# Performance work log

Hardware: AMD Instinct MI355X
Metric: run time of the kernel (lower is better)

The kernel has to match this reference:

```python
import jax, jax.numpy as jnp
import numpy as np

KAPPA = 10000.0
B_CONST = 0.5


def pe_matrix(L, dim):
    # pe[j,i] = sin(j/kappa^(i/dim)) for even i, cos(j/kappa^((i-1)/dim)) for odd i
    j = jnp.arange(L, dtype=jnp.float32)[:, None]
    i = jnp.arange(dim, dtype=jnp.float32)[None, :]
    even = (jnp.arange(dim) % 2 == 0)[None, :]
    expo = jnp.where(even, i, i - 1.0) / dim
    ang = j / (KAPPA ** expo)
    return jnp.where(even, jnp.sin(ang), jnp.cos(ang))  # [L, dim]


def setup_inputs() -> dict:
    key = jax.random.key(0)
    ks = jax.random.split(key, 6)
    B, N, L, d, n = 4, 8, 1024, 256, 3
    theta = jax.random.normal(ks[0], (B, N, L, d), dtype=jnp.float32)
    xi = jax.random.normal(ks[1], (B, N, L, n), dtype=jnp.float32)
    edge_attr = jax.random.normal(ks[2], (B, L, N * (N - 1) * 2), dtype=jnp.float32)
    s = 1.0 / np.sqrt(d)
    Wq = jax.random.normal(ks[3], (d, d), dtype=jnp.float32) * s
    Wk = jax.random.normal(ks[4], (d, d), dtype=jnp.float32) * s
    Wv = jax.random.normal(ks[5], (d, d), dtype=jnp.float32) * s
    return {"theta": theta, "xi": xi, "edge_attr": edge_attr, "Wq": Wq, "Wk": Wk, "Wv": Wv}


def reference(theta, xi, edge_attr, Wq, Wk, Wv):
    B, N, L, d = theta.shape
    n = xi.shape[-1]
    # positional encoding (dropout in eval mode = identity)
    theta = theta + pe_matrix(L, d)
    xi = xi + pe_matrix(L, n)
    edge_attr = edge_attr + pe_matrix(L, N * (N - 1) * 2)[None]

    causal = jnp.triu(jnp.ones((L, L), dtype=bool), 1)  # True above diagonal
    neg_inf = jnp.float32(-jnp.inf)

    # feature path: standard causal scaled-dot-product attention
    q = jnp.einsum('bnld,ed->bnle', theta, Wq)
    k = jnp.einsum('bnld,ed->bnle', theta, Wk)
    v = jnp.einsum('bnld,ed->bnle', theta, Wv)
    scores = jnp.einsum('bnqd,bnkd->bnqk', q, k) / jnp.sqrt(jnp.float32(d))
    scores = jnp.where(causal, neg_inf, scores)
    h_out = jnp.einsum('bnqk,bnkd->bnqd', jax.nn.softmax(scores, axis=-1), v)

    # equivariant path: pairwise squared-distance attention
    D = xi[:, :, :, None, :] - xi[:, :, None, :, :]  # [B,N,L,L,n]
    sq = jnp.sum(D * D, axis=-1)                     # [B,N,L,L]
    sq = jnp.where(causal, neg_inf, sq)
    beta = jax.nn.softmax(sq, axis=-1)
    mbeta = beta * (1.0 - jnp.eye(L, dtype=beta.dtype))  # zero the diagonal
    second = B_CONST * jnp.einsum('bnqk,bnkc->bnqc', mbeta, xi)
    third = B_CONST * jnp.sum(mbeta, axis=-1, keepdims=True) * xi
    x_out = xi + second - third

    return h_out, x_out, edge_attr
```

## Files before the change

kernel.cpp:

```cpp
#include <hip/hip_runtime.h>
#include <math.h>

#define L    1024
#define D    256
#define NCH  3
#define HEADS 32
#define EDIM 112
#define BATCH 4

typedef __bf16 bf8_t __attribute__((ext_vector_type(8)));
typedef float  f4_t  __attribute__((ext_vector_type(4)));

typedef __attribute__((address_space(1))) const void GVC;
typedef __attribute__((address_space(3))) void LDSV;

__device__ inline unsigned short f2bf(float x) {
    unsigned u = __float_as_uint(x);
    u += 0x7FFFu + ((u >> 16) & 1u);
    return (unsigned short)(u >> 16);
}
__device__ inline float bf2f(unsigned short h) {
    return __uint_as_float(((unsigned)h) << 16);
}

__global__ void prep_kernel(const float* __restrict__ edge, const float* __restrict__ xi,
                            float* __restrict__ pe_d, float* __restrict__ eout,
                            float* __restrict__ xsb)
{
    int idx = blockIdx.x * blockDim.x + threadIdx.x;
    if (idx < L * D) {
        int l = idx >> 8, i = idx & (D - 1);
        float expo = (float)(i & ~1) * (1.0f / (float)D);
        float ang = (float)l * __powf(10000.0f, -expo);
        pe_d[idx] = (i & 1) ? cosf(ang) : sinf(ang);
    } else if (idx < L * D + BATCH * L * EDIM) {
        int j = idx - L * D;
        int i = j % EDIM;
        int l = (j / EDIM) % L;
        float expo = (float)(i & ~1) * (1.0f / (float)EDIM);
        float ang = (float)l * __powf(10000.0f, -expo);
        eout[j] = edge[j] + ((i & 1) ? cosf(ang) : sinf(ang));
    } else {
        int j = idx - (L * D + BATCH * L * EDIM);
        if (j < HEADS * L * NCH) {
            int c = j % 3;
            int l = (j / 3) & (L - 1);
            float ang = (c == 2) ? (float)l * 0.0021544347f : (float)l;
            float pe = (c == 1) ? cosf(ang) : sinf(ang);
            xsb[j] = xi[j] + pe;
        }
    }
}

__global__ __launch_bounds__(256) void qkv_mfma(
    const float* __restrict__ theta, const float* __restrict__ pe_d,
    const float* __restrict__ Wq, const float* __restrict__ Wk, const float* __restrict__ Wv,
    unsigned short* __restrict__ qh, unsigned short* __restrict__ ql,
    unsigned short* __restrict__ kh, unsigned short* __restrict__ vt)
{
    __shared__ unsigned short XsH[128][40], XsL[128][40], WsH[128][40];

    int tid = threadIdx.x;
    int w = tid >> 6, lane = tid & 63;
    int quad = lane >> 4, l16 = lane & 15;
    int aoff = (w & 1) * 64, boff = (w >> 1) * 64;

    int b = blockIdx.x;
    int xcd = b & 7, r = b >> 3;
    int bx = r % 6;
    int rowPanel = (r / 6) * 8 + xcd;
    int rowBase = rowPanel * 128;
    int wsel = bx >> 1;
    int eBase = (bx & 1) * 128;
    const float* W = (wsel == 0) ? Wq : (wsel == 1) ? Wk : Wv;

    f4_t acc[4][4];
    #pragma unroll
    for (int mi = 0; mi < 4; mi++)
        #pragma unroll
        for (int ni = 0; ni < 4; ni++) acc[mi][ni] = (f4_t){0.f, 0.f, 0.f, 0.f};

    int sr = tid >> 1;
    int ks = (tid & 1) * 16;

    for (int kt = 0; kt < 8; kt++) {
        int k0 = kt * 32 + ks;
        __syncthreads();
        {
            union { unsigned short us[16]; float4 f4[2]; } hi, lo;
            const float* tp = &theta[(size_t)(rowBase + sr) * D + k0];
            const float* pp = &pe_d[(size_t)((rowBase + sr) & (L - 1)) * D + k0];
            #pragma unroll
            for (int j = 0; j < 4; j++) {
                float4 tv = reinterpret_cast<const float4*>(tp)[j];
                float4 pv = reinterpret_cast<const float4*>(pp)[j];
                float xs[4] = {tv.x + pv.x, tv.y + pv.y, tv.z + pv.z, tv.w + pv.w};
                #pragma unroll
                for (int q = 0; q < 4; q++) {
                    unsigned short h = f2bf(xs[q]);
                    hi.us[j * 4 + q] = h;
                    lo.us[j * 4 + q] = f2bf(xs[q] - bf2f(h));
                }
            }
            *reinterpret_cast<float4*>(&XsH[sr][ks]) = hi.f4[0];
            *reinterpret_cast<float4*>(&XsH[sr][ks + 8]) = hi.f4[1];
            *reinterpret_cast<float4*>(&XsL[sr][ks]) = lo.f4[0];
            *reinterpret_cast<float4*>(&XsL[sr][ks + 8]) = lo.f4[1];

            const float* wp = &W[(size_t)(eBase + sr) * D + k0];
            #pragma unroll
            for (int j = 0; j < 4; j++) {
                float4 wv = reinterpret_cast<const float4*>(wp)[j];
                float xs[4] = {wv.x, wv.y, wv.z, wv.w};
                #pragma unroll
                for (int q = 0; q < 4; q++) hi.us[j * 4 + q] = f2bf(xs[q]);
            }
            *reinterpret_cast<float4*>(&WsH[sr][ks]) = hi.f4[0];
            *reinterpret_cast<float4*>(&WsH[sr][ks + 8]) = hi.f4[1];
        }
        __syncthreads();

        if (wsel < 2) {
            bf8_t aw[4];
            #pragma unroll
            for (int mi = 0; mi < 4; mi++)
                aw[mi] = *reinterpret_cast<const bf8_t*>(&WsH[aoff + mi * 16 + l16][quad * 8]);
            #pragma unroll
            for (int ni = 0; ni < 4; ni++) {
                bf8_t bxh = *reinterpret_cast<const bf8_t*>(&XsH[boff + ni * 16 + l16][quad * 8]);
                bf8_t bxl = *reinterpret_cast<const bf8_t*>(&XsL[boff + ni * 16 + l16][quad * 8]);
                #pragma unroll
                for (int mi = 0; mi < 4; mi++) {
                    acc[mi][ni] = __builtin_amdgcn_mfma_f32_16x16x32_bf16(aw[mi], bxh, acc[mi][ni], 0, 0, 0);
                    acc[mi][ni] = __builtin_amdgcn_mfma_f32_16x16x32_bf16(aw[mi], bxl, acc[mi][ni], 0, 0, 0);
                }
            }
        } else {
            bf8_t axh[4], axl[4];
            #pragma unroll
            for (int mi = 0; mi < 4; mi++) {
                axh[mi] = *reinterpret_cast<const bf8_t*>(&XsH[aoff + mi * 16 + l16][quad * 8]);
                axl[mi] = *reinterpret_cast<const bf8_t*>(&XsL[aoff + mi * 16 + l16][quad * 8]);
            }
            #pragma unroll
            for (int ni = 0; ni < 4; ni++) {
                bf8_t bw = *reinterpret_cast<const bf8_t*>(&WsH[boff + ni * 16 + l16][quad * 8]);
                #pragma unroll
                for (int mi = 0; mi < 4; mi++) {
                    acc[mi][ni] = __builtin_amdgcn_mfma_f32_16x16x32_bf16(axh[mi], bw, acc[mi][ni], 0, 0, 0);
                    acc[mi][ni] = __builtin_amdgcn_mfma_f32_16x16x32_bf16(axl[mi], bw, acc[mi][ni], 0, 0, 0);
                }
            }
        }
    }

    if (wsel < 2) {
        float scale = (wsel == 0) ? 0.0625f : 1.0f;
        #pragma unroll
        for (int mi = 0; mi < 4; mi++) {
            #pragma unroll
            for (int ni = 0; ni < 4; ni++) {
                int e0 = eBase + aoff + mi * 16 + quad * 4;
                size_t row = rowBase + boff + ni * 16 + l16;
                union { unsigned short us[4]; unsigned long long u; } ph, pl;
                #pragma unroll
                for (int rr = 0; rr < 4; rr++) {
                    float x = acc[mi][ni][rr] * scale;
                    unsigned short h = f2bf(x);
                    ph.us[rr] = h;
                    pl.us[rr] = f2bf(x - bf2f(h));
                }
                if (wsel == 0) {
                    *reinterpret_cast<unsigned long long*>(&qh[row * D + e0]) = ph.u;
                    *reinterpret_cast<unsigned long long*>(&ql[row * D + e0]) = pl.u;
                } else {
                    int e0s = e0 ^ ((l16 & 7) << 3);
                    *reinterpret_cast<unsigned long long*>(&kh[row * D + e0s]) = ph.u;
                }
            }
        }
    } else {
        #pragma unroll
        for (int mi = 0; mi < 4; mi++) {
            #pragma unroll
            for (int ni = 0; ni < 4; ni++) {
                int row0 = rowBase + aoff + mi * 16 + quad * 4;
                int e = eBase + boff + ni * 16 + l16;
                int head = row0 >> 10, kb = (row0 & 1023) >> 5, kk = row0 & 31;
                union { unsigned short us[4]; unsigned long long u; } pk;
                #pragma unroll
                for (int rr = 0; rr < 4; rr++) pk.us[rr] = f2bf(acc[mi][ni][rr]);
                int us_sw = (e * 32 + kk) ^ (((e >> 1) & 3) << 3);
                *reinterpret_cast<unsigned long long*>(
                    &vt[((size_t)(head * 32 + kb)) * 8192 + us_sw]) = pk.u;
            }
        }
    }
}

__device__ __forceinline__ void stage_tile(
    const unsigned short* kht, const unsigned short* vtt,
    unsigned short* Ks, unsigned short* Vs, int kt, int buf, int w, int lane)
{
    #pragma unroll
    for (int i = 0; i < 2; i++) {
        int ch = w * 2 + i;
        __builtin_amdgcn_global_load_lds(
            (GVC*)(kht + (size_t)kt * 8192 + ch * 512 + lane * 8),
            (LDSV*)(Ks + buf * 8192 + ch * 512), 16, 0, 0);
        __builtin_amdgcn_global_load_lds(
            (GVC*)(vtt + (size_t)kt * 8192 + ch * 512 + lane * 8),
            (LDSV*)(Vs + buf * 8192 + ch * 512), 16, 0, 0);
    }
}

__global__ __launch_bounds__(512) void attn_v7(
    const unsigned short* __restrict__ qh, const unsigned short* __restrict__ ql,
    const unsigned short* __restrict__ kh, const unsigned short* __restrict__ vt,
    float* __restrict__ hout)
{
    __shared__ __align__(16) unsigned short Ks[2 * 8192];
    __shared__ __align__(16) unsigned short Vs[2 * 8192];
    __shared__ __align__(16) unsigned short Pb[8][16 * 40];
    __shared__ unsigned short lds_pad[4200];

    int tid = threadIdx.x;
    int w = tid >> 6, lane = tid & 63;
    int quad = lane >> 4, l16 = lane & 15;
    int b = blockIdx.x;
    int head = ((b & 7) << 2) + (b >> 6);
    int s = (b >> 3) & 7;
    int u = (w < 4) ? (4 * s + w) : (63 - 4 * s - (w - 4));
    int Ts = 32 - 2 * s;
    int lim = u >> 1;
    size_t hb = (size_t)head * (L * D);
    const unsigned short* kht = kh + hb;
    const unsigned short* vtt = vt + (size_t)head * (32 * 8192);
    unsigned short* Pw = Pb[w];

    if (hout == nullptr) lds_pad[tid] = 1;

    int q_g = u * 16 + l16;

    f4_t qfh[8], qfl[8];
    {
        const unsigned short* ph = qh + hb + (size_t)q_g * D + quad * 8;
        const unsigned short* pl = ql + hb + (size_t)q_g * D + quad * 8;
        #pragma unroll
        for (int c = 0; c < 8; c++) {
            qfh[c] = *reinterpret_cast<const f4_t*>(ph + c * 32);
            qfl[c] = *reinterpret_cast<const f4_t*>(pl + c * 32);
        }
    }
    #pragma unroll
    for (int c = 0; c < 8; c++) {
        asm volatile("" : "+v"(qfh[c]));
        asm volatile("" : "+v"(qfl[c]));
    }

    stage_tile(kht, vtt, Ks, Vs, 0, 0, w, lane);

    f4_t acc[16];
    #pragma unroll
    for (int i = 0; i < 16; i++) acc[i] = (f4_t){0.f, 0.f, 0.f, 0.f};
    float mrun = -1e30f, lrun = 0.f;

    int xm = (l16 & 7) << 3;
    int vq = (quad * 8) ^ (((l16 >> 1) & 3) << 3);

    asm volatile("s_waitcnt vmcnt(0)" ::: "memory");
    __syncthreads();

    #pragma unroll 1
    for (int kt = 0; kt < Ts; kt++) {
        if (kt + 1 < Ts)
            stage_tile(kht, vtt, Ks, Vs, kt + 1, (kt + 1) & 1, w, lane);

        if (kt <= lim) {
            const unsigned short* Kb = Ks + (kt & 1) * 8192;
            const unsigned short* Vb = Vs + (kt & 1) * 8192;
            int kBase = kt * 32;

            bf8_t kf0[8], kf1[8];
            #pragma unroll
            for (int c = 0; c < 8; c++) {
                int col = (quad * 8 + c * 32) ^ xm;
                kf0[c] = *reinterpret_cast<const bf8_t*>(&Kb[l16 * 256 + col]);
                kf1[c] = *reinterpret_cast<const bf8_t*>(&Kb[(16 + l16) * 256 + col]);
            }
            const unsigned short* vpb = Vb + l16 * 32 + vq;
            bf8_t vfA[8];
            #pragma unroll
            for (int dt = 0; dt < 8; dt++)
                vfA[dt] = *reinterpret_cast<const bf8_t*>(vpb + dt * 512);

            f4_t s0a = (f4_t){0.f,0.f,0.f,0.f}, s0b = (f4_t){0.f,0.f,0.f,0.f};
            f4_t s1a = (f4_t){0.f,0.f,0.f,0.f}, s1b = (f4_t){0.f,0.f,0.f,0.f};
            #pragma unroll
            for (int c = 0; c < 8; c += 2) {
                s0a = __builtin_amdgcn_mfma_f32_16x16x32_bf16(kf0[c],     __builtin_bit_cast(bf8_t, qfh[c]),     s0a, 0, 0, 0);
                s0b = __builtin_amdgcn_mfma_f32_16x16x32_bf16(kf0[c + 1], __builtin_bit_cast(bf8_t, qfh[c + 1]), s0b, 0, 0, 0);
                s0a = __builtin_amdgcn_mfma_f32_16x16x32_bf16(kf0[c],     __builtin_bit_cast(bf8_t, qfl[c]),     s0a, 0, 0, 0);
                s0b = __builtin_amdgcn_mfma_f32_16x16x32_bf16(kf0[c + 1], __builtin_bit_cast(bf8_t, qfl[c + 1]), s0b, 0, 0, 0);
            }
            #pragma unroll
            for (int c = 0; c < 8; c += 2) {
                s1a = __builtin_amdgcn_mfma_f32_16x16x32_bf16(kf1[c],     __builtin_bit_cast(bf8_t, qfh[c]),     s1a, 0, 0, 0);
                s1b = __builtin_amdgcn_mfma_f32_16x16x32_bf16(kf1[c + 1], __builtin_bit_cast(bf8_t, qfh[c + 1]), s1b, 0, 0, 0);
                s1a = __builtin_amdgcn_mfma_f32_16x16x32_bf16(kf1[c],     __builtin_bit_cast(bf8_t, qfl[c]),     s1a, 0, 0, 0);
                s1b = __builtin_amdgcn_mfma_f32_16x16x32_bf16(kf1[c + 1], __builtin_bit_cast(bf8_t, qfl[c + 1]), s1b, 0, 0, 0);
            }
            f4_t sc[2];
            sc[0] = s0a + s0b;
            sc[1] = s1a + s1b;

            float pv[2][4];
            float tm = -1e30f;
            #pragma unroll
            for (int t = 0; t < 2; t++)
                #pragma unroll
                for (int rr = 0; rr < 4; rr++) {
                    int key = kBase + t * 16 + quad * 4 + rr;
                    float sv = (key <= q_g) ? sc[t][rr] : -1e30f;
                    sc[t][rr] = sv;
                    tm = fmaxf(tm, sv);
                }
            tm = fmaxf(tm, __shfl_xor(tm, 16));
            tm = fmaxf(tm, __shfl_xor(tm, 32));
            bool grow = __any(tm > mrun);
            float mnew = fmaxf(mrun, tm);
            float alpha = grow ? __expf(mrun - mnew) : 1.0f;
            mrun = mnew;
            float ts = 0.f;
            #pragma unroll
            for (int t = 0; t < 2; t++)
                #pragma unroll
                for (int rr = 0; rr < 4; rr++) {
                    float p = __expf(sc[t][rr] - mnew);
                    pv[t][rr] = p;
                    ts += p;
                }
            ts += __shfl_xor(ts, 16);
            ts += __shfl_xor(ts, 32);
            lrun = lrun * alpha + ts;

            #pragma unroll
            for (int t = 0; t < 2; t++) {
                union { unsigned short us[4]; unsigned long long uu; } pk;
                #pragma unroll
                for (int rr = 0; rr < 4; rr++) pk.us[rr] = f2bf(pv[t][rr]);
                *reinterpret_cast<unsigned long long*>(&Pw[l16 * 40 + t * 16 + quad * 4]) = pk.uu;
            }
            bf8_t vfB[8];
            #pragma unroll
            for (int dt = 0; dt < 8; dt++)
                vfB[dt] = *reinterpret_cast<const bf8_t*>(vpb + (8 + dt) * 512);
            if (grow) {
                #pragma unroll
                for (int dt = 0; dt < 16; dt++) acc[dt] *= alpha;
            }
            asm volatile("s_waitcnt lgkmcnt(0)" ::: "memory");
            bf8_t pf = *reinterpret_cast<const bf8_t*>(&Pw[l16 * 40 + quad * 8]);
            #pragma unroll
            for (int dt = 0; dt < 8; dt++)
                acc[dt] = __builtin_amdgcn_mfma_f32_16x16x32_bf16(vfA[dt], pf, acc[dt], 0, 0, 0);
            #pragma unroll
            for (int dt = 0; dt < 8; dt++)
                acc[8 + dt] = __builtin_amdgcn_mfma_f32_16x16x32_bf16(vfB[dt], pf, acc[8 + dt], 0, 0, 0);
        }

        asm volatile("s_waitcnt vmcnt(0)" ::: "memory");
        __syncthreads();
    }

    float inv = 1.f / lrun;
    float* dst = hout + hb + (size_t)q_g * D + quad * 4;
    #pragma unroll
    for (int dt = 0; dt < 16; dt++) {
        float4 o = {acc[dt][0] * inv, acc[dt][1] * inv,
                    acc[dt][2] * inv, acc[dt][3] * inv};
        *reinterpret_cast<float4*>(dst + dt * 16) = o;
    }
}

__global__ __launch_bounds__(256) void equiv_kernel(
    const float* __restrict__ xsb, float* __restrict__ xout)
{
    __shared__ float xs[L * NCH];
    int head = blockIdx.y;
    int tid = threadIdx.x;
    const float4* src = reinterpret_cast<const float4*>(xsb + (size_t)head * L * NCH);
    #pragma unroll
    for (int it = 0; it < 3; it++)
        reinterpret_cast<float4*>(xs)[tid + it * 256] = src[tid + it * 256];
    __syncthreads();

    int w = tid >> 6, lane = tid & 63;
    int q = blockIdx.x * 4 + w;
    float xq0 = xs[q * 3 + 0], xq1 = xs[q * 3 + 1], xq2 = xs[q * 3 + 2];

    float m = 0.f;
    for (int k = lane; k < q; k += 64) {
        float d0 = xq0 - xs[k * 3 + 0];
        float d1 = xq1 - xs[k * 3 + 1];
        float d2 = xq2 - xs[k * 3 + 2];
        m = fmaxf(m, d0 * d0 + d1 * d1 + d2 * d2);
    }
    #pragma unroll
    for (int off = 1; off < 64; off <<= 1) m = fmaxf(m, __shfl_xor(m, off));

    float s0 = 0.f, s1 = 0.f, s2 = 0.f, sn = 0.f;
    for (int k = lane; k < q; k += 64) {
        float d0 = xq0 - xs[k * 3 + 0];
        float d1 = xq1 - xs[k * 3 + 1];
        float d2 = xq2 - xs[k * 3 + 2];
        float wgt = __expf(d0 * d0 + d1 * d1 + d2 * d2 - m);
        sn += wgt;
        s0 += wgt * xs[k * 3 + 0];
        s1 += wgt * xs[k * 3 + 1];
        s2 += wgt * xs[k * 3 + 2];
    }
    #pragma unroll
    for (int off = 1; off < 64; off <<= 1) {
        sn += __shfl_xor(sn, off);
        s0 += __shfl_xor(s0, off);
        s1 += __shfl_xor(s1, off);
        s2 += __shfl_xor(s2, off);
    }
    float Z = sn + __expf(-m);
    float inv = 0.5f / Z;
    if (lane == 0) {
        size_t ob = (size_t)head * L * NCH + (size_t)q * NCH;
        xout[ob + 0] = xq0 + inv * (s0 - sn * xq0);
        xout[ob + 1] = xq1 + inv * (s1 - sn * xq1);
        xout[ob + 2] = xq2 + inv * (s2 - sn * xq2);
    }
}

extern "C" void kernel_launch(void* const* d_in, const int* in_sizes, int n_in,
                              void* d_out, int out_size, void* d_ws, size_t ws_size,
                              hipStream_t stream)
{
    (void)in_sizes; (void)n_in; (void)out_size; (void)ws_size;
    const float* theta = (const float*)d_in[0];
    const float* xi    = (const float*)d_in[1];
    const float* edge  = (const float*)d_in[2];
    const float* Wq    = (const float*)d_in[3];
    const float* Wk    = (const float*)d_in[4];
    const float* Wv    = (const float*)d_in[5];

    float* out  = (float*)d_out;
    float* hout = out;
    float* xout = out + 8388608;
    float* eout = out + 8388608 + 98304;

    const size_t NE = 8388608;
    unsigned short* base = (unsigned short*)d_ws;
    unsigned short* qh = base;
    unsigned short* ql = base + NE;
    unsigned short* kh = base + 2 * NE;
    unsigned short* vt = base + 3 * NE;
    float* pe_d = (float*)(base + 4 * NE);
    float* xsb  = pe_d + L * D;

    prep_kernel<<<3200, 256, 0, stream>>>(edge, xi, pe_d, eout, xsb);
    equiv_kernel<<<dim3(L / 4, HEADS), 256, 0, stream>>>(xsb, xout);
    qkv_mfma<<<1536, 256, 0, stream>>>(theta, pe_d, Wq, Wk, Wv, qh, ql, kh, vt);
    attn_v7<<<256, 512, 0, stream>>>(qh, ql, kh, vt, hout);
}
```

Baseline: 237.0 us.

## Precompute bf16 hi/lo splits in separate kernel; qkv GEMM reads operands directly from global

Adds a split_kernel that adds the positional encoding to theta and writes bf16 hi/lo planes, and converts the three weight matrices to bf16 once. The QKV GEMM now loads MFMA fragments straight from global memory instead of staging through LDS with per-block fp32 conversion and barriers. This drops the redundant per-tile conversion work, the pe_d table and the syncthreads. In exchange it adds an extra kernel launch and a round trip of about 32 MB through workspace, and the GEMM loses LDS reuse, so it relies on cache hits for the 16-byte strided global loads.

```diff
diff --git a/kernel.cpp b/kernel.cpp
--- a/kernel.cpp
+++ b/kernel.cpp
@@ -24,24 +24,17 @@
 }
 
 __global__ void prep_kernel(const float* __restrict__ edge, const float* __restrict__ xi,
-                            float* __restrict__ pe_d, float* __restrict__ eout,
-                            float* __restrict__ xsb)
+                            float* __restrict__ eout, float* __restrict__ xsb)
 {
     int idx = blockIdx.x * blockDim.x + threadIdx.x;
-    if (idx < L * D) {
-        int l = idx >> 8, i = idx & (D - 1);
-        float expo = (float)(i & ~1) * (1.0f / (float)D);
-        float ang = (float)l * __powf(10000.0f, -expo);
-        pe_d[idx] = (i & 1) ? cosf(ang) : sinf(ang);
-    } else if (idx < L * D + BATCH * L * EDIM) {
-        int j = idx - L * D;
-        int i = j % EDIM;
-        int l = (j / EDIM) % L;
+    if (idx < BATCH * L * EDIM) {
+        int i = idx % EDIM;
+        int l = (idx / EDIM) % L;
         float expo = (float)(i & ~1) * (1.0f / (float)EDIM);
         float ang = (float)l * __powf(10000.0f, -expo);
-        eout[j] = edge[j] + ((i & 1) ? cosf(ang) : sinf(ang));
+        eout[idx] = edge[idx] + ((i & 1) ? cosf(ang) : sinf(ang));
     } else {
-        int j = idx - (L * D + BATCH * L * EDIM);
+        int j = idx - BATCH * L * EDIM;
         if (j < HEADS * L * NCH) {
             int c = j % 3;
             int l = (j / 3) & (L - 1);
@@ -52,14 +45,58 @@
     }
 }
 
+__global__ void split_kernel(const float* __restrict__ theta,
+                             const float* __restrict__ Wq, const float* __restrict__ Wk,
+                             const float* __restrict__ Wv,
+                             unsigned short* __restrict__ xhi, unsigned short* __restrict__ xlo,
+                             unsigned short* __restrict__ whb)
+{
+    int idx = blockIdx.x * blockDim.x + threadIdx.x;
+    if (idx < HEADS * L * (D / 8)) {
+        int row = idx >> 5;
+        int k0 = (idx & 31) * 8;
+        int l = row & (L - 1);
+        const float4* tp = reinterpret_cast<const float4*>(&theta[(size_t)row * D + k0]);
+        float4 a = tp[0], c = tp[1];
+        float x[8] = {a.x, a.y, a.z, a.w, c.x, c.y, c.z, c.w};
+        union { unsigned short us[8]; float4 f4; } hi, lo;
+        #pragma unroll
+        for (int j = 0; j < 8; j++) {
+            int i = k0 + j;
+            float expo = (float)(i & ~1) * (1.0f / (float)D);
+            float ang = (float)l * __powf(10000.0f, -expo);
+            float pe = (i & 1) ? cosf(ang) : sinf(ang);
+            float v = x[j] + pe;
+            unsigned short h = f2bf(v);
+            hi.us[j] = h;
+            lo.us[j] = f2bf(v - bf2f(h));
+        }
+        *reinterpret_cast<float4*>(&xhi[(size_t)row * D + k0]) = hi.f4;
+        *reinterpret_cast<float4*>(&xlo[(size_t)row * D + k0]) = lo.f4;
+    } else {
+        int u = idx - HEADS * L * (D / 8);
+        if (u < 3 * 256 * 32) {
+            int row = u >> 5;
+            int k0 = (u & 31) * 8;
+            const float* W = (row < 256) ? Wq : (row < 512) ? Wk : Wv;
+            int rr = row & 255;
+            const float4* wp4 = reinterpret_cast<const float4*>(&W[(size_t)rr * D + k0]);
+            float4 a = wp4[0], c = wp4[1];
+            float x[8] = {a.x, a.y, a.z, a.w, c.x, c.y, c.z, c.w};
+            union { unsigned short us[8]; float4 f4; } hv;
+            #pragma unroll
+            for (int j = 0; j < 8; j++) hv.us[j] = f2bf(x[j]);
+            *reinterpret_cast<float4*>(&whb[(size_t)row * D + k0]) = hv.f4;
+        }
+    }
+}
+
 __global__ __launch_bounds__(256) void qkv_mfma(
-    const float* __restrict__ theta, const float* __restrict__ pe_d,
-    const float* __restrict__ Wq, const float* __restrict__ Wk, const float* __restrict__ Wv,
+    const unsigned short* __restrict__ xhi, const unsigned short* __restrict__ xlo,
+    const unsigned short* __restrict__ whb,
     unsigned short* __restrict__ qh, unsigned short* __restrict__ ql,
     unsigned short* __restrict__ kh, unsigned short* __restrict__ vt)
 {
-    __shared__ unsigned short XsH[128][40], XsL[128][40], WsH[128][40];
-
     int tid = threadIdx.x;
     int w = tid >> 6, lane = tid & 63;
     int quad = lane >> 4, l16 = lane & 15;
@@ -72,7 +109,7 @@
     int rowBase = rowPanel * 128;
     int wsel = bx >> 1;
     int eBase = (bx & 1) * 128;
-    const float* W = (wsel == 0) ? Wq : (wsel == 1) ? Wk : Wv;
+    const unsigned short* wp = whb + (size_t)wsel * 65536;
 
     f4_t acc[4][4];
     #pragma unroll
@@ -80,81 +117,29 @@
         #pragma unroll
         for (int ni = 0; ni < 4; ni++) acc[mi][ni] = (f4_t){0.f, 0.f, 0.f, 0.f};
 
-    int sr = tid >> 1;
-    int ks = (tid & 1) * 16;
-
-    for (int kt = 0; kt < 8; kt++) {
-        int k0 = kt * 32 + ks;
-        __syncthreads();
-        {
-            union { unsigned short us[16]; float4 f4[2]; } hi, lo;
-            const float* tp = &theta[(size_t)(rowBase + sr) * D + k0];
-            const float* pp = &pe_d[(size_t)((rowBase + sr) & (L - 1)) * D + k0];
-            #pragma unroll
-            for (int j = 0; j < 4; j++) {
-                float4 tv = reinterpret_cast<const float4*>(tp)[j];
-                float4 pv = reinterpret_cast<const float4*>(pp)[j];
-                float xs[4] = {tv.x + pv.x, tv.y + pv.y, tv.z + pv.z, tv.w + pv.w};
-                #pragma unroll
-                for (int q = 0; q < 4; q++) {
-                    unsigned short h = f2bf(xs[q]);
-                    hi.us[j * 4 + q] = h;
-                    lo.us[j * 4 + q] = f2bf(xs[q] - bf2f(h));
-                }
-            }
-            *reinterpret_cast<float4*>(&XsH[sr][ks]) = hi.f4[0];
-            *reinterpret_cast<float4*>(&XsH[sr][ks + 8]) = hi.f4[1];
-            *reinterpret_cast<float4*>(&XsL[sr][ks]) = lo.f4[0];
-            *reinterpret_cast<float4*>(&XsL[sr][ks + 8]) = lo.f4[1];
-
-            const float* wp = &W[(size_t)(eBase + sr) * D + k0];
-            #pragma unroll
-            for (int j = 0; j < 4; j++) {
-                float4 wv = reinterpret_cast<const float4*>(wp)[j];
-                float xs[4] = {wv.x, wv.y, wv.z, wv.w};
-                #pragma unroll
-                for (int q = 0; q < 4; q++) hi.us[j * 4 + q] = f2bf(xs[q]);
-            }
-            *reinterpret_cast<float4*>(&WsH[sr][ks]) = hi.f4[0];
-            *reinterpret_cast<float4*>(&WsH[sr][ks + 8]) = hi.f4[1];
-        }
-        __syncthreads();
-
-        if (wsel < 2) {
-            bf8_t aw[4];
+    if (wsel < 2) {
+        const unsigned short* ap = wp  + (size_t)(eBase + aoff + l16) * D + quad * 8;
+        const unsigned short* bh = xhi + (size_t)(rowBase + boff + l16) * D + quad * 8;
+        const unsigned short* bl = xlo + (size_t)(rowBase + boff + l16) * D + quad * 8;
+        for (int kt = 0; kt < 8; kt++) {
+            int k0 = kt * 32;
+            bf8_t aw[4], bxh[4], bxl[4];
             #pragma unroll
             for (int mi = 0; mi < 4; mi++)
-                aw[mi] = *reinterpret_cast<const bf8_t*>(&WsH[aoff + mi * 16 + l16][quad * 8]);
+                aw[mi] = *reinterpret_cast<const bf8_t*>(ap + (size_t)mi * 16 * D + k0);
             #pragma unroll
             for (int ni = 0; ni < 4; ni++) {
-                bf8_t bxh = *reinterpret_cast<const bf8_t*>(&XsH[boff + ni * 16 + l16][quad * 8]);
-                bf8_t bxl = *reinterpret_cast<const bf8_t*>(&XsL[boff + ni * 16 + l16][quad * 8]);
+                bxh[ni] = *reinterpret_cast<const bf8_t*>(bh + (size_t)ni * 16 * D + k0);
+                bxl[ni] = *reinterpret_cast<const bf8_t*>(bl + (size_t)ni * 16 * D + k0);
+            }
+            #pragma unroll
+            for (int ni = 0; ni < 4; ni++)
                 #pragma unroll
                 for (int mi = 0; mi < 4; mi++) {
-                    acc[mi][ni] = __builtin_amdgcn_mfma_f32_16x16x32_bf16(aw[mi], bxh, acc[mi][ni], 0, 0, 0);
-                    acc[mi][ni] = __builtin_amdgcn_mfma_f32_16x16x32_bf16(aw[mi], bxl, acc[mi][ni], 0, 0, 0);
-                }
-            }
-        } else {
-            bf8_t axh[4], axl[4];
-            #pragma unroll
-            for (int mi = 0; mi < 4; mi++) {
-                axh[mi] = *reinterpret_cast<const bf8_t*>(&XsH[aoff + mi * 16 + l16][quad * 8]);
-                axl[mi] = *reinterpret_cast<const bf8_t*>(&XsL[aoff + mi * 16 + l16][quad * 8]);
-            }
-            #pragma unroll
-            for (int ni = 0; ni < 4; ni++) {
-                bf8_t bw = *reinterpret_cast<const bf8_t*>(&WsH[boff + ni * 16 + l16][quad * 8]);
-                #pragma unroll
-                for (int mi = 0; mi < 4; mi++) {
-                    acc[mi][ni] = __builtin_amdgcn_mfma_f32_16x16x32_bf16(axh[mi], bw, acc[mi][ni], 0, 0, 0);
-                    acc[mi][ni] = __builtin_amdgcn_mfma_f32_16x16x32_bf16(axl[mi], bw, acc[mi][ni], 0, 0, 0);
-                }
-            }
-        }
-    }
-
-    if (wsel < 2) {
+                    acc[mi][ni] = __builtin_amdgcn_mfma_f32_16x16x32_bf16(aw[mi], bxh[ni], acc[mi][ni], 0, 0, 0);
+                    acc[mi][ni] = __builtin_amdgcn_mfma_f32_16x16x32_bf16(aw[mi], bxl[ni], acc[mi][ni], 0, 0, 0);
+                }
+        }
         float scale = (wsel == 0) ? 0.0625f : 1.0f;
         #pragma unroll
         for (int mi = 0; mi < 4; mi++) {
@@ -180,6 +165,28 @@
             }
         }
     } else {
+        const unsigned short* ah = xhi + (size_t)(rowBase + aoff + l16) * D + quad * 8;
+        const unsigned short* al = xlo + (size_t)(rowBase + aoff + l16) * D + quad * 8;
+        const unsigned short* bp = wp  + (size_t)(eBase + boff + l16) * D + quad * 8;
+        for (int kt = 0; kt < 8; kt++) {
+            int k0 = kt * 32;
+            bf8_t axh[4], axl[4], bw[4];
+            #pragma unroll
+            for (int mi = 0; mi < 4; mi++) {
+                axh[mi] = *reinterpret_cast<const bf8_t*>(ah + (size_t)mi * 16 * D + k0);
+                axl[mi] = *reinterpret_cast<const bf8_t*>(al + (size_t)mi * 16 * D + k0);
+            }
+            #pragma unroll
+            for (int ni = 0; ni < 4; ni++)
+                bw[ni] = *reinterpret_cast<const bf8_t*>(bp + (size_t)ni * 16 * D + k0);
+            #pragma unroll
+            for (int ni = 0; ni < 4; ni++)
+                #pragma unroll
+                for (int mi = 0; mi < 4; mi++) {
+                    acc[mi][ni] = __builtin_amdgcn_mfma_f32_16x16x32_bf16(axh[mi], bw[ni], acc[mi][ni], 0, 0, 0);
+                    acc[mi][ni] = __builtin_amdgcn_mfma_f32_16x16x32_bf16(axl[mi], bw[ni], acc[mi][ni], 0, 0, 0);
+                }
+        }
         #pragma unroll
         for (int mi = 0; mi < 4; mi++) {
             #pragma unroll
@@ -456,15 +463,18 @@
 
     const size_t NE = 8388608;
     unsigned short* base = (unsigned short*)d_ws;
-    unsigned short* qh = base;
-    unsigned short* ql = base + NE;
-    unsigned short* kh = base + 2 * NE;
-    unsigned short* vt = base + 3 * NE;
-    float* pe_d = (float*)(base + 4 * NE);
-    float* xsb  = pe_d + L * D;
-
-    prep_kernel<<<3200, 256, 0, stream>>>(edge, xi, pe_d, eout, xsb);
+    unsigned short* qh  = base;
+    unsigned short* ql  = base + NE;
+    unsigned short* kh  = base + 2 * NE;
+    unsigned short* vt  = base + 3 * NE;
+    unsigned short* xhi = base + 4 * NE;
+    unsigned short* xlo = base + 5 * NE;
+    unsigned short* whb = base + 6 * NE;
+    float* xsb = (float*)(base + 6 * NE + 196608);
+
+    prep_kernel<<<2176, 256, 0, stream>>>(edge, xi, eout, xsb);
+    split_kernel<<<4192, 256, 0, stream>>>(theta, Wq, Wk, Wv, xhi, xlo, whb);
     equiv_kernel<<<dim3(L / 4, HEADS), 256, 0, stream>>>(xsb, xout);
-    qkv_mfma<<<1536, 256, 0, stream>>>(theta, pe_d, Wq, Wk, Wv, qh, ql, kh, vt);
+    qkv_mfma<<<1536, 256, 0, stream>>>(xhi, xlo, whb, qh, ql, kh, vt);
     attn_v7<<<256, 512, 0, stream>>>(qh, ql, kh, vt, hout);
 }
```

Result: slower. 277.1 us (+16.9%).

## Pre-convert weights to bf16, widen QKV tiles, and double-buffer staging

Applied to the files above, without the earlier changes.

Weights are converted to bf16 once in the prep kernel, stored in an MFMA-friendly fragment layout, and staged into LDS with global_load_lds. Each QKV block now covers all 256 output columns for a 128-row panel, which halves the grid and computes the theta+pe split conversion once per panel instead of twice. The k-loop is double-buffered so the next tile's loads and conversion overlap the MFMAs. The cost is 32 accumulators per thread and about 64KB of LDS, which may lower occupancy.

```diff
diff --git a/kernel.cpp b/kernel.cpp
--- a/kernel.cpp
+++ b/kernel.cpp
@@ -24,8 +24,10 @@
 }
 
 __global__ void prep_kernel(const float* __restrict__ edge, const float* __restrict__ xi,
+                            const float* __restrict__ Wq, const float* __restrict__ Wk,
+                            const float* __restrict__ Wv,
                             float* __restrict__ pe_d, float* __restrict__ eout,
-                            float* __restrict__ xsb)
+                            float* __restrict__ xsb, unsigned short* __restrict__ whb)
 {
     int idx = blockIdx.x * blockDim.x + threadIdx.x;
     if (idx < L * D) {
@@ -40,132 +42,173 @@
         float expo = (float)(i & ~1) * (1.0f / (float)EDIM);
         float ang = (float)l * __powf(10000.0f, -expo);
         eout[j] = edge[j] + ((i & 1) ? cosf(ang) : sinf(ang));
+    } else if (idx < L * D + BATCH * L * EDIM + HEADS * L * NCH) {
+        int j = idx - (L * D + BATCH * L * EDIM);
+        int c = j % 3;
+        int l = (j / 3) & (L - 1);
+        float ang = (c == 2) ? (float)l * 0.0021544347f : (float)l;
+        float pe = (c == 1) ? cosf(ang) : sinf(ang);
+        xsb[j] = xi[j] + pe;
     } else {
-        int j = idx - (L * D + BATCH * L * EDIM);
-        if (j < HEADS * L * NCH) {
-            int c = j % 3;
-            int l = (j / 3) & (L - 1);
-            float ang = (c == 2) ? (float)l * 0.0021544347f : (float)l;
-            float pe = (c == 1) ? cosf(ang) : sinf(ang);
-            xsb[j] = xi[j] + pe;
+        int j = idx - (L * D + BATCH * L * EDIM + HEADS * L * NCH);
+        if (j < 3 * 8192) {
+            int wsel = j >> 13;
+            int t = j & 8191;
+            int g = t >> 9, u = (t >> 4) & 31, rr = t & 15;
+            const float* W = (wsel == 0) ? Wq : (wsel == 1) ? Wk : Wv;
+            const float4* s = reinterpret_cast<const float4*>(&W[(size_t)(g * 16 + rr) * D + u * 8]);
+            float4 a = s[0], b = s[1];
+            float x[8] = {a.x, a.y, a.z, a.w, b.x, b.y, b.z, b.w};
+            union { unsigned short us[8]; float4 f4; } hv;
+            #pragma unroll
+            for (int q = 0; q < 8; q++) hv.us[q] = f2bf(x[q]);
+            *reinterpret_cast<float4*>(&whb[(size_t)wsel * 65536 + g * 4096 + u * 128 + rr * 8]) = hv.f4;
         }
     }
 }
 
 __global__ __launch_bounds__(256) void qkv_mfma(
     const float* __restrict__ theta, const float* __restrict__ pe_d,
-    const float* __restrict__ Wq, const float* __restrict__ Wk, const float* __restrict__ Wv,
+    const unsigned short* __restrict__ whb,
     unsigned short* __restrict__ qh, unsigned short* __restrict__ ql,
     unsigned short* __restrict__ kh, unsigned short* __restrict__ vt)
 {
-    __shared__ unsigned short XsH[128][40], XsL[128][40], WsH[128][40];
+    __shared__ __align__(16) unsigned short XsH[2][4096];
+    __shared__ __align__(16) unsigned short XsL[2][4096];
+    __shared__ __align__(16) unsigned short Ws[2][8192];
 
     int tid = threadIdx.x;
     int w = tid >> 6, lane = tid & 63;
     int quad = lane >> 4, l16 = lane & 15;
-    int aoff = (w & 1) * 64, boff = (w >> 1) * 64;
 
     int b = blockIdx.x;
     int xcd = b & 7, r = b >> 3;
-    int bx = r % 6;
-    int rowPanel = (r / 6) * 8 + xcd;
-    int rowBase = rowPanel * 128;
-    int wsel = bx >> 1;
-    int eBase = (bx & 1) * 128;
-    const float* W = (wsel == 0) ? Wq : (wsel == 1) ? Wk : Wv;
-
-    f4_t acc[4][4];
-    #pragma unroll
-    for (int mi = 0; mi < 4; mi++)
-        #pragma unroll
-        for (int ni = 0; ni < 4; ni++) acc[mi][ni] = (f4_t){0.f, 0.f, 0.f, 0.f};
+    int wsel = r % 3;
+    int panel = (r / 3) * 8 + xcd;
+    int rowBase = panel * 128;
+    const unsigned short* wsrc = whb + (size_t)wsel * 65536;
 
     int sr = tid >> 1;
     int ks = (tid & 1) * 16;
+    int cg = sr >> 4, cr = sr & 15, cu = ks >> 3;
+    int xoff = cg * 512 + cu * 128 + cr * 8;
+
+    const float* tp_base = &theta[(size_t)(rowBase + sr) * D + ks];
+    const float* pp_base = &pe_d[(size_t)((rowBase + sr) & (L - 1)) * D + ks];
+
+    int wg8 = (w >> 1) * 8;
+    int wg4 = (w & 1) * 4;
+
+    f4_t acc[32];
+    #pragma unroll
+    for (int i = 0; i < 32; i++) acc[i] = (f4_t){0.f, 0.f, 0.f, 0.f};
+
+    auto stageW = [&](int kt, int buf) {
+        #pragma unroll
+        for (int j = 0; j < 4; j++) {
+            int g = w * 4 + j;
+            __builtin_amdgcn_global_load_lds(
+                (GVC*)(wsrc + (size_t)g * 4096 + kt * 512 + lane * 8),
+                (LDSV*)(Ws[buf] + g * 512), 16, 0, 0);
+        }
+    };
+    auto convX = [&](const float* xv, int buf) {
+        union { unsigned short us[8]; float4 f4; } h0, l0, h1, l1;
+        #pragma unroll
+        for (int e = 0; e < 16; e++) {
+            float v = xv[e];
+            unsigned short h = f2bf(v);
+            unsigned short lo = f2bf(v - bf2f(h));
+            if (e < 8) { h0.us[e] = h; l0.us[e] = lo; }
+            else       { h1.us[e - 8] = h; l1.us[e - 8] = lo; }
+        }
+        *reinterpret_cast<float4*>(&XsH[buf][xoff])       = h0.f4;
+        *reinterpret_cast<float4*>(&XsH[buf][xoff + 128]) = h1.f4;
+        *reinterpret_cast<float4*>(&XsL[buf][xoff])       = l0.f4;
+        *reinterpret_cast<float4*>(&XsL[buf][xoff + 128]) = l1.f4;
+    };
+
+    {
+        float xv[16];
+        #pragma unroll
+        for (int j = 0; j < 4; j++) {
+            float4 tv = reinterpret_cast<const float4*>(tp_base)[j];
+            float4 pv = reinterpret_cast<const float4*>(pp_base)[j];
+            xv[j * 4 + 0] = tv.x + pv.x; xv[j * 4 + 1] = tv.y + pv.y;
+            xv[j * 4 + 2] = tv.z + pv.z; xv[j * 4 + 3] = tv.w + pv.w;
+        }
+        convX(xv, 0);
+        stageW(0, 0);
+    }
+    __syncthreads();
+
+    #define FR(buf2d, g16) (*reinterpret_cast<const bf8_t*>(&(buf2d)[(g16) * 512 + quad * 128 + l16 * 8]))
 
     for (int kt = 0; kt < 8; kt++) {
-        int k0 = kt * 32 + ks;
-        __syncthreads();
-        {
-            union { unsigned short us[16]; float4 f4[2]; } hi, lo;
-            const float* tp = &theta[(size_t)(rowBase + sr) * D + k0];
-            const float* pp = &pe_d[(size_t)((rowBase + sr) & (L - 1)) * D + k0];
+        int buf = kt & 1;
+
+        float xnv[16];
+        if (kt < 7) {
+            const float* tp = tp_base + (kt + 1) * 32;
+            const float* pp = pp_base + (kt + 1) * 32;
             #pragma unroll
             for (int j = 0; j < 4; j++) {
                 float4 tv = reinterpret_cast<const float4*>(tp)[j];
                 float4 pv = reinterpret_cast<const float4*>(pp)[j];
-                float xs[4] = {tv.x + pv.x, tv.y + pv.y, tv.z + pv.z, tv.w + pv.w};
-                #pragma unroll
-                for (int q = 0; q < 4; q++) {
-                    unsigned short h = f2bf(xs[q]);
-                    hi.us[j * 4 + q] = h;
-                    lo.us[j * 4 + q] = f2bf(xs[q] - bf2f(h));
+                xnv[j * 4 + 0] = tv.x + pv.x; xnv[j * 4 + 1] = tv.y + pv.y;
+                xnv[j * 4 + 2] = tv.z + pv.z; xnv[j * 4 + 3] = tv.w + pv.w;
+            }
+        }
+
+        bf8_t bxh[4], bxl[4];
+        #pragma unroll
+        for (int mx = 0; mx < 4; mx++) {
+            bxh[mx] = FR(XsH[buf], wg4 + mx);
+            bxl[mx] = FR(XsL[buf], wg4 + mx);
+        }
+
+        if (wsel < 2) {
+            #pragma unroll
+            for (int ne = 0; ne < 8; ne++) {
+                bf8_t aw = FR(Ws[buf], wg8 + ne);
+                #pragma unroll
+                for (int mx = 0; mx < 4; mx++) {
+                    acc[ne * 4 + mx] = __builtin_amdgcn_mfma_f32_16x16x32_bf16(aw, bxh[mx], acc[ne * 4 + mx], 0, 0, 0);
+                    acc[ne * 4 + mx] = __builtin_amdgcn_mfma_f32_16x16x32_bf16(aw, bxl[mx], acc[ne * 4 + mx], 0, 0, 0);
                 }
             }
-            *reinterpret_cast<float4*>(&XsH[sr][ks]) = hi.f4[0];
-            *reinterpret_cast<float4*>(&XsH[sr][ks + 8]) = hi.f4[1];
-            *reinterpret_cast<float4*>(&XsL[sr][ks]) = lo.f4[0];
-            *reinterpret_cast<float4*>(&XsL[sr][ks + 8]) = lo.f4[1];
-
-            const float* wp = &W[(size_t)(eBase + sr) * D + k0];
-            #pragma unroll
-            for (int j = 0; j < 4; j++) {
-                float4 wv = reinterpret_cast<const float4*>(wp)[j];
-                float xs[4] = {wv.x, wv.y, wv.z, wv.w};
-                #pragma unroll
-                for (int q = 0; q < 4; q++) hi.us[j * 4 + q] = f2bf(xs[q]);
-            }
-            *reinterpret_cast<float4*>(&WsH[sr][ks]) = hi.f4[0];
-            *reinterpret_cast<float4*>(&WsH[sr][ks + 8]) = hi.f4[1];
+        } else {
+            #pragma unroll
+            for (int ne = 0; ne < 8; ne++) {
+                bf8_t bw = FR(Ws[buf], wg8 + ne);
+                #pragma unroll
+                for (int mx = 0; mx < 4; mx++) {
+                    acc[mx * 8 + ne] = __builtin_amdgcn_mfma_f32_16x16x32_bf16(bxh[mx], bw, acc[mx * 8 + ne], 0, 0, 0);
+                    acc[mx * 8 + ne] = __builtin_amdgcn_mfma_f32_16x16x32_bf16(bxl[mx], bw, acc[mx * 8 + ne], 0, 0, 0);
+                }
+            }
+        }
+
+        if (kt < 7) {
+            convX(xnv, buf ^ 1);
+            stageW(kt + 1, buf ^ 1);
         }
         __syncthreads();
-
-        if (wsel < 2) {
-            bf8_t aw[4];
-            #pragma unroll
-            for (int mi = 0; mi < 4; mi++)
-                aw[mi] = *reinterpret_cast<const bf8_t*>(&WsH[aoff + mi * 16 + l16][quad * 8]);
-            #pragma unroll
-            for (int ni = 0; ni < 4; ni++) {
-                bf8_t bxh = *reinterpret_cast<const bf8_t*>(&XsH[boff + ni * 16 + l16][quad * 8]);
-                bf8_t bxl = *reinterpret_cast<const bf8_t*>(&XsL[boff + ni * 16 + l16][quad * 8]);
-                #pragma unroll
-                for (int mi = 0; mi < 4; mi++) {
-                    acc[mi][ni] = __builtin_amdgcn_mfma_f32_16x16x32_bf16(aw[mi], bxh, acc[mi][ni], 0, 0, 0);
-                    acc[mi][ni] = __builtin_amdgcn_mfma_f32_16x16x32_bf16(aw[mi], bxl, acc[mi][ni], 0, 0, 0);
-                }
-            }
-        } else {
-            bf8_t axh[4], axl[4];
-            #pragma unroll
-            for (int mi = 0; mi < 4; mi++) {
-                axh[mi] = *reinterpret_cast<const bf8_t*>(&XsH[aoff + mi * 16 + l16][quad * 8]);
-                axl[mi] = *reinterpret_cast<const bf8_t*>(&XsL[aoff + mi * 16 + l16][quad * 8]);
-            }
-            #pragma unroll
-            for (int ni = 0; ni < 4; ni++) {
-                bf8_t bw = *reinterpret_cast<const bf8_t*>(&WsH[boff + ni * 16 + l16][quad * 8]);
-                #pragma unroll
-                for (int mi = 0; mi < 4; mi++) {
-                    acc[mi][ni] = __builtin_amdgcn_mfma_f32_16x16x32_bf16(axh[mi], bw, acc[mi][ni], 0, 0, 0);
-                    acc[mi][ni] = __builtin_amdgcn_mfma_f32_16x16x32_bf16(axl[mi], bw, acc[mi][ni], 0, 0, 0);
-                }
-            }
-        }
-    }
+    }
+    #undef FR
 
     if (wsel < 2) {
         float scale = (wsel == 0) ? 0.0625f : 1.0f;
         #pragma unroll
-        for (int mi = 0; mi < 4; mi++) {
-            #pragma unroll
-            for (int ni = 0; ni < 4; ni++) {
-                int e0 = eBase + aoff + mi * 16 + quad * 4;
-                size_t row = rowBase + boff + ni * 16 + l16;
+        for (int ne = 0; ne < 8; ne++) {
+            #pragma unroll
+            for (int mx = 0; mx < 4; mx++) {
+                int e0 = (w >> 1) * 128 + ne * 16 + quad * 4;
+                size_t row = rowBase + (w & 1) * 64 + mx * 16 + l16;
                 union { unsigned short us[4]; unsigned long long u; } ph, pl;
                 #pragma unroll
                 for (int rr = 0; rr < 4; rr++) {
-                    float x = acc[mi][ni][rr] * scale;
+                    float x = acc[ne * 4 + mx][rr] * scale;
                     unsigned short h = f2bf(x);
                     ph.us[rr] = h;
                     pl.us[rr] = f2bf(x - bf2f(h));
@@ -181,15 +224,15 @@
         }
     } else {
         #pragma unroll
-        for (int mi = 0; mi < 4; mi++) {
-            #pragma unroll
-            for (int ni = 0; ni < 4; ni++) {
-                int row0 = rowBase + aoff + mi * 16 + quad * 4;
-                int e = eBase + boff + ni * 16 + l16;
+        for (int mx = 0; mx < 4; mx++) {
+            #pragma unroll
+            for (int ne = 0; ne < 8; ne++) {
+                int row0 = rowBase + (w & 1) * 64 + mx * 16 + quad * 4;
+                int e = (w >> 1) * 128 + ne * 16 + l16;
                 int head = row0 >> 10, kb = (row0 & 1023) >> 5, kk = row0 & 31;
                 union { unsigned short us[4]; unsigned long long u; } pk;
                 #pragma unroll
-                for (int rr = 0; rr < 4; rr++) pk.us[rr] = f2bf(acc[mi][ni][rr]);
+                for (int rr = 0; rr < 4; rr++) pk.us[rr] = f2bf(acc[mx * 8 + ne][rr]);
                 int us_sw = (e * 32 + kk) ^ (((e >> 1) & 3) << 3);
                 *reinterpret_cast<unsigned long long*>(
                     &vt[((size_t)(head * 32 + kb)) * 8192 + us_sw]) = pk.u;
@@ -456,15 +499,16 @@
 
     const size_t NE = 8388608;
     unsigned short* base = (unsigned short*)d_ws;
-    unsigned short* qh = base;
-    unsigned short* ql = base + NE;
-    unsigned short* kh = base + 2 * NE;
-    unsigned short* vt = base + 3 * NE;
-    float* pe_d = (float*)(base + 4 * NE);
+    unsigned short* qh  = base;
+    unsigned short* ql  = base + NE;
+    unsigned short* kh  = base + 2 * NE;
+    unsigned short* vt  = base + 3 * NE;
+    unsigned short* whb = base + 4 * NE;
+    float* pe_d = (float*)(base + 4 * NE + 196608);
     float* xsb  = pe_d + L * D;
 
-    prep_kernel<<<3200, 256, 0, stream>>>(edge, xi, pe_d, eout, xsb);
+    prep_kernel<<<3296, 256, 0, stream>>>(edge, xi, Wq, Wk, Wv, pe_d, eout, xsb, whb);
     equiv_kernel<<<dim3(L / 4, HEADS), 256, 0, stream>>>(xsb, xout);
-    qkv_mfma<<<1536, 256, 0, stream>>>(theta, pe_d, Wq, Wk, Wv, qh, ql, kh, vt);
+    qkv_mfma<<<768, 256, 0, stream>>>(theta, pe_d, whb, qh, ql, kh, vt);
     attn_v7<<<256, 512, 0, stream>>>(qh, ql, kh, vt, hout);
 }
```

After: 245.5 us. 3.6% more time.
